# Optimization experiments

Measured on AMD Instinct MI355X. Metric: run time of the kernel, lower is better.

Reference implementation:

```python
import jax, jax.numpy as jnp
import numpy as np

B, N, D_MODEL, H = 2, 512, 256, 8
DH, DS, DE = 8, 8, 8          # hyperbolic / spherical / euclidean component dims
HEAD = D_MODEL // H           # 32
HALF = HEAD // 2              # 16 rope frequencies
KAPPA_S = 1.0                 # spherical curvature
EPS = 1e-6


def setup_inputs() -> dict:
    key = jax.random.key(0)
    ks = jax.random.split(key, 10)
    h = jax.random.normal(ks[0], (B, N, D_MODEL), jnp.float32)
    # manifold coords: hyperbolic part inside Poincare ball, spherical part on unit sphere
    xh = 0.3 * jnp.tanh(jax.random.normal(ks[1], (B, N, DH), jnp.float32))
    xs_raw = jax.random.normal(ks[2], (B, N, DS), jnp.float32)
    xs = xs_raw / jnp.linalg.norm(xs_raw, axis=-1, keepdims=True)
    xe = jax.random.normal(ks[3], (B, N, DE), jnp.float32)
    x = jnp.concatenate([xh, xs, xe], axis=-1)
    def lin(k):
        return 0.05 * jax.random.normal(k, (D_MODEL, D_MODEL), jnp.float32)
    inp = dict(
        h=h, x=x,
        Wq=lin(ks[4]), bq=jnp.zeros((D_MODEL,), jnp.float32),
        Wk=lin(ks[5]), bk=jnp.zeros((D_MODEL,), jnp.float32),
        Wv=lin(ks[6]), bv=jnp.zeros((D_MODEL,), jnp.float32),
        Wo=lin(ks[7]), bo=jnp.zeros((D_MODEL,), jnp.float32),
        w_kernel=jnp.ones((H, 3), jnp.float32),   # torch init: ones(num_heads, num_comp)
        beta=jnp.ones((H,), jnp.float32),
        edge_bias=0.1 * jax.random.normal(ks[8], (B, 1, N, N), jnp.float32),
        node_mask=jnp.ones((B, N), bool),
    )
    return inp


def _pairwise_geometry(x):
    """Returns dh (B,N,N), sdot (B,N,N), de2 (B,N,N), dist (B,N,N)."""
    xh, xs, xe = x[..., :DH], x[..., DH:DH + DS], x[..., DH + DS:]
    # hyperbolic: Poincare-ball distance arccosh(1 + 2|a-b|^2 / ((1-|a|^2)(1-|b|^2)))
    dh2_num = jnp.sum((xh[:, :, None, :] - xh[:, None, :, :]) ** 2, -1)
    one_m = 1.0 - jnp.sum(xh * xh, -1)                               # (B,N)
    arg = 1.0 + 2.0 * dh2_num / (one_m[:, :, None] * one_m[:, None, :])
    dh = jnp.arccosh(jnp.maximum(arg, 1.0 + EPS))
    # spherical: arccos of dot (unit vectors); raw dot kept for the kernel term
    sdot = jnp.einsum('bnd,bmd->bnm', xs, xs)
    ds = jnp.arccos(jnp.clip(sdot, -1.0 + EPS, 1.0 - EPS)) / np.sqrt(KAPPA_S)
    # euclidean: squared distance (kernel uses -d^2; product dist uses d^2)
    de2 = jnp.sum((xe[:, :, None, :] - xe[:, None, :, :]) ** 2, -1)
    dist = jnp.sqrt(dh * dh + ds * ds + de2)
    return dh, sdot, de2, dist


def reference(h, x, Wq, bq, Wk, bk, Wv, bv, Wo, bo, w_kernel, beta, edge_bias, node_mask):
    scale = 1.0 / np.sqrt(HEAD)
    rope_freq = jnp.exp(-np.log(10000.0) * jnp.arange(HALF, dtype=jnp.float32) / HALF)

    def heads(t):  # (B,N,D) -> (B,H,N,head)
        return t.reshape(B, N, H, HEAD).transpose(0, 2, 1, 3)

    Q = heads(h @ Wq.T + bq)
    K = heads(h @ Wk.T + bk)
    V = heads(h @ Wv.T + bv)

    dh, sdot, de2, dist = _pairwise_geometry(x)

    # M-RoPE: rotate Q by pairwise angle theta_ij = omega * d_M(x_i, x_j)
    theta = dist[..., None] * rope_freq                  # (B,N,N,half)
    cos_t = jnp.cos(theta)[:, None]                      # (B,1,N,N,half)
    sin_t = jnp.sin(theta)[:, None]
    q1, q2 = Q[..., 0::2], Q[..., 1::2]                  # (B,H,N,half)
    k1, k2 = K[..., 0::2], K[..., 1::2]
    qk_same = q1[:, :, :, None, :] * k1[:, :, None, :, :] + q2[:, :, :, None, :] * k2[:, :, None, :, :]
    qk_cross = q1[:, :, :, None, :] * k2[:, :, None, :, :] - q2[:, :, :, None, :] * k1[:, :, None, :, :]
    attn = (cos_t * qk_same + sin_t * qk_cross).sum(-1) * scale   # (B,H,N,N)

    # geodesic kernel bias: per-component kernels [H:-d_H, S:k*a.b, E:-|a-b|^2]
    kernel_stack = jnp.stack([-dh, KAPPA_S * sdot, -de2], axis=-1)  # (B,N,N,3)
    geo = jnp.einsum('hc,bnmc->bhnm', w_kernel, kernel_stack)
    attn = attn + beta[None, :, None, None] * geo + edge_bias

    attn = jnp.where(node_mask[:, None, None, :], attn, -jnp.inf)
    p = jax.nn.softmax(attn, axis=-1)
    out = jnp.einsum('bhnm,bhmd->bhnd', p, V).transpose(0, 2, 1, 3).reshape(B, N, D_MODEL)
    return out @ Wo.T + bo
```

## Files before the change

kernel.cpp:

```cpp
#include <hip/hip_runtime.h>

#define N_TOK 512
#define NH 8

typedef __attribute__((ext_vector_type(8))) short short8;
typedef __attribute__((ext_vector_type(4))) short short4v;
typedef __attribute__((ext_vector_type(4))) float f32x4;
typedef __attribute__((ext_vector_type(2))) _Float16 half2v;
typedef __attribute__((ext_vector_type(4))) _Float16 half4v;
typedef __attribute__((ext_vector_type(8))) _Float16 half8v;

__device__ __forceinline__ unsigned short f2bf(float f) {
    union { float f; unsigned u; } v; v.f = f;
    return (unsigned short)((v.u + 0x7FFF + ((v.u >> 16) & 1)) >> 16);
}

__global__ __launch_bounds__(256) void gemm_qkv_mfma(
    const float* __restrict__ A, const float* __restrict__ x,
    const float* __restrict__ Wq, const float* __restrict__ Wk, const float* __restrict__ Wv,
    const float* __restrict__ bq, const float* __restrict__ bk, const float* __restrict__ bv,
    float* __restrict__ Qb, _Float16* __restrict__ KT2, float* __restrict__ Vb,
    float* __restrict__ xT)
{
    const int bx = blockIdx.x;
    const int t = threadIdx.x;
    if (bx >= 768) {
        int idx = bx - 768;
        int b = idx / 24, k = idx % 24;
        const float* src = x + (size_t)b * 512 * 24 + k;
        float* dst = xT + (size_t)b * 12288 + k * 512;
        for (int j = t; j < 512; j += 256) dst[j] = src[j * 24];
        return;
    }
    const int z = bx >> 8, rem = bx & 255;
    const int m0 = (rem >> 3) * 32, n0 = (rem & 7) * 32;
    const float* W    = (z == 0) ? Wq : (z == 1) ? Wk : Wv;
    const float* bias = (z == 0) ? bq : (z == 1) ? bk : bv;

    __shared__ short As[32][264];
    __shared__ short Ws[32][264];

    #pragma unroll
    for (int r = 0; r < 8; ++r) {
        int idx = t + 256 * r;
        int row = idx >> 6, c4 = (idx & 63) * 4;
        float4 a = *(const float4*)&A[(m0 + row) * 256 + c4];
        short4v pa = {(short)f2bf(a.x), (short)f2bf(a.y), (short)f2bf(a.z), (short)f2bf(a.w)};
        *(short4v*)&As[row][c4] = pa;
        float4 w = *(const float4*)&W[(n0 + row) * 256 + c4];
        short4v pw = {(short)f2bf(w.x), (short)f2bf(w.y), (short)f2bf(w.z), (short)f2bf(w.w)};
        *(short4v*)&Ws[row][c4] = pw;
    }
    __syncthreads();

    const int w = t >> 6, lane = t & 63;
    const int wm = (w >> 1) * 16, wn = (w & 1) * 16;
    const int frow = lane & 15, kq = lane >> 4;

    f32x4 acc = {0.f, 0.f, 0.f, 0.f};
    #pragma unroll
    for (int k0 = 0; k0 < 8; ++k0) {
        short8 af = *(const short8*)&As[wm + frow][k0 * 32 + kq * 8];
        short8 wf = *(const short8*)&Ws[wn + frow][k0 * 32 + kq * 8];
        if (z == 1) acc = __builtin_amdgcn_mfma_f32_16x16x32_bf16(wf, af, acc, 0, 0, 0);
        else        acc = __builtin_amdgcn_mfma_f32_16x16x32_bf16(af, wf, acc, 0, 0, 0);
    }
    const int col = lane & 15, rq = (lane >> 4) * 4;
    if (z == 1) {
        int tok = m0 + wm + col;
        int bb = tok >> 9, jloc = tok & 511;
        #pragma unroll
        for (int r = 0; r < 4; ++r) {
            int d = n0 + wn + rq + r;
            KT2[(size_t)bb * 131072 + (size_t)(d >> 1) * 1024 + jloc * 2 + (d & 1)]
                = (_Float16)(acc[r] + bias[d]);
        }
    } else {
        float* C = (z == 0) ? Qb : Vb;
        const float sc = (z == 0) ? 0.17677669529663687f : 1.0f;
        float bsv = bias[n0 + wn + col];
        #pragma unroll
        for (int r = 0; r < 4; ++r)
            C[(m0 + wm + rq + r) * 256 + n0 + wn + col] = (acc[r] + bsv) * sc;
    }
}

__global__ __launch_bounds__(512, 4) void attn_kernel(
    const float* __restrict__ Q, const _Float16* __restrict__ KT2, const float* __restrict__ V,
    const float* __restrict__ x, const float* __restrict__ xT,
    const float* __restrict__ wker, const float* __restrict__ beta,
    const float* __restrict__ eb, float* __restrict__ Ao)
{
    const int i0 = blockIdx.x * 2;
    const int b  = blockIdx.y;
    const int t  = threadIdx.x;
    const int lane = t & 63;
    const int h = __builtin_amdgcn_readfirstlane(t >> 6);

    __shared__ half8v csn[16][2][64];
    __shared__ float es[2][NH][128];
    __shared__ float gdh[2][512], gsd[2][512], gde[2][512], gdist[2][512];

    {
        const float* xc = xT + (size_t)b * 12288 + t;
        float xv[24];
        #pragma unroll
        for (int k = 0; k < 24; ++k) xv[k] = xc[k * 512];
        float oj = 0.f;
        #pragma unroll
        for (int k = 0; k < 8; ++k) oj += xv[k] * xv[k];
        #pragma unroll
        for (int p = 0; p < 2; ++p) {
            const float* xi = x + (size_t)(b * N_TOK + i0 + p) * 24;
            float onemi = 1.0f, dh2 = 0.f, sd = 0.f, de2 = 0.f;
            #pragma unroll
            for (int k = 0; k < 8; ++k) {
                onemi -= xi[k] * xi[k];
                float d = xi[k] - xv[k]; dh2 += d * d;
            }
            #pragma unroll
            for (int k = 0; k < 8; ++k) sd += xi[8 + k] * xv[8 + k];
            #pragma unroll
            for (int k = 0; k < 8; ++k) { float d = xi[16 + k] - xv[16 + k]; de2 += d * d; }
            float arg = fmaf(2.0f * dh2, __builtin_amdgcn_rcpf(onemi * (1.0f - oj)), 1.0f);
            arg = fmaxf(arg, 1.0f + 1e-6f);
            float dh = __logf(arg + __builtin_amdgcn_sqrtf(fmaf(arg, arg, -1.0f)));
            float sdc = fminf(fmaxf(sd, -1.0f + 1e-6f), 1.0f - 1e-6f);
            float ax = fabsf(sdc);
            float pp = fmaf(ax, -0.0012624911f, 0.0066700901f);
            pp = fmaf(pp, ax, -0.0170881256f);
            pp = fmaf(pp, ax,  0.0308918810f);
            pp = fmaf(pp, ax, -0.0501743046f);
            pp = fmaf(pp, ax,  0.0889789874f);
            pp = fmaf(pp, ax, -0.2145988016f);
            pp = fmaf(pp, ax,  1.5707963050f);
            pp *= __builtin_amdgcn_sqrtf(1.0f - ax);
            float dsp = (sdc < 0.f) ? (3.14159265358979f - pp) : pp;
            float dist = __builtin_amdgcn_sqrtf(fmaf(dh, dh, fmaf(dsp, dsp, de2)));
            gdh[p][t] = dh; gsd[p][t] = sd; gde[p][t] = de2; gdist[p][t] = dist;
        }
    }

    const float* q0p = Q + (size_t)(b * N_TOK + i0) * 256 + h * 32;
    const float* q1p = q0p + 256;
    const float bet = beta[h];
    const float bw0 = bet * wker[h * 3 + 0], bw1 = bet * wker[h * 3 + 1], bw2 = bet * wker[h * 3 + 2];

    const int gjj = t & 127;
    const int gfh = __builtin_amdgcn_readfirstlane((t >> 7) & 1);
    const int gii = __builtin_amdgcn_readfirstlane(t >> 8);
    float frq[8];
    #pragma unroll
    for (int r = 0; r < 8; ++r)
        frq[r] = __expf(-0.5756462732485115f * (float)(gfh * 8 + r));

    float dsum[2] = {0.f, 0.f};
    float accv[2][4] = {{0.f,0.f,0.f,0.f},{0.f,0.f,0.f,0.f}};
    const int jsub = lane >> 3, dq = lane & 7;

    auto build = [&](int tile) {
        float d = gdist[gii][tile * 128 + gjj];
        #pragma unroll
        for (int r = 0; r < 8; ++r) {
            float sv, cv;
            __sincosf(d * frq[r], &sv, &cv);
            half4v p;
            p[0] = (_Float16)cv; p[1] = (_Float16)sv;
            p[2] = (_Float16)(-sv); p[3] = (_Float16)cv;
            ((half4v*)&csn[gfh * 8 + r][gii][gjj >> 1])[gjj & 1] = p;
        }
    };

    __syncthreads();
    build(0);
    const float* ebp0 = eb + ((size_t)b * N_TOK + i0) * N_TOK + 2 * lane;
    const float* ebp1 = ebp0 + N_TOK;
    float2 ebn0 = *(const float2*)ebp0;
    float2 ebn1 = *(const float2*)ebp1;
    __syncthreads();

    const _Float16* kbase = KT2 + (size_t)b * 131072 + (size_t)(h * 16) * 1024 + 4 * lane;

    for (int tile = 0; tile < 4; ++tile) {
        float2 eb0 = ebn0, eb1 = ebn1;
        if (tile < 3) {
            ebn0 = *(const float2*)(ebp0 + (tile + 1) * 128);
            ebn1 = *(const float2*)(ebp1 + (tile + 1) * 128);
        }
        {
            const _Float16* kp = kbase + tile * 256;
            half4v karr[16];
            #pragma unroll
            for (int f = 0; f < 16; ++f) karr[f] = *(const half4v*)(kp + f * 1024);

            float dot[2][2] = {{0.f, 0.f}, {0.f, 0.f}};
            #pragma unroll
            for (int f = 0; f < 16; ++f) {
                half2v k0 = {karr[f][0], karr[f][1]};
                half2v k1 = {karr[f][2], karr[f][3]};
                float q10 = q0p[2 * f], q20 = q0p[2 * f + 1];
                float q11 = q1p[2 * f], q21 = q1p[2 * f + 1];
                #pragma unroll
                for (int ii = 0; ii < 2; ++ii) {
                    half8v c8 = csn[f][ii][lane];
                    half2v cs0 = {c8[0], c8[1]}, rt0 = {c8[2], c8[3]};
                    half2v cs1 = {c8[4], c8[5]}, rt1 = {c8[6], c8[7]};
#if __has_builtin(__builtin_amdgcn_fdot2)
                    float u0 = __builtin_amdgcn_fdot2(cs0, k0, 0.f, false);
                    float v0 = __builtin_amdgcn_fdot2(rt0, k0, 0.f, false);
                    float u1 = __builtin_amdgcn_fdot2(cs1, k1, 0.f, false);
                    float v1 = __builtin_amdgcn_fdot2(rt1, k1, 0.f, false);
#else
                    float u0 = (float)cs0[0]*(float)k0[0] + (float)cs0[1]*(float)k0[1];
                    float v0 = (float)rt0[0]*(float)k0[0] + (float)rt0[1]*(float)k0[1];
                    float u1 = (float)cs1[0]*(float)k1[0] + (float)cs1[1]*(float)k1[1];
                    float v1 = (float)rt1[0]*(float)k1[0] + (float)rt1[1]*(float)k1[1];
#endif
                    float qa = ii ? q11 : q10, qb = ii ? q21 : q20;
                    dot[ii][0] = fmaf(qa, u0, fmaf(qb, v0, dot[ii][0]));
                    dot[ii][1] = fmaf(qa, u1, fmaf(qb, v1, dot[ii][1]));
                }
            }
            #pragma unroll
            for (int ii = 0; ii < 2; ++ii) {
                float2 g1 = *(const float2*)&gdh[ii][tile * 128 + 2 * lane];
                float2 g2 = *(const float2*)&gsd[ii][tile * 128 + 2 * lane];
                float2 g3 = *(const float2*)&gde[ii][tile * 128 + 2 * lane];
                float2 e2 = ii ? eb1 : eb0;
                float s0 = dot[ii][0] + (bw1 * g2.x - bw0 * g1.x - bw2 * g3.x) + e2.x;
                float s1 = dot[ii][1] + (bw1 * g2.y - bw0 * g1.y - bw2 * g3.y) + e2.y;
                float e0 = __expf(s0), e1 = __expf(s1);
                dsum[ii] += e0 + e1;
                *(float2*)&es[ii][h][2 * lane] = make_float2(e0, e1);
            }
        }
        if (tile < 3) { __syncthreads(); build(tile + 1); }
        {
            const float* vp = V + (size_t)(b * N_TOK + tile * 128 + jsub) * 256 + h * 32 + dq * 4;
            #pragma unroll
            for (int it = 0; it < 16; ++it) {
                float4 v4 = *(const float4*)(vp + it * 8 * 256);
                float e0 = es[0][h][it * 8 + jsub], e1 = es[1][h][it * 8 + jsub];
                accv[0][0] += e0 * v4.x; accv[0][1] += e0 * v4.y;
                accv[0][2] += e0 * v4.z; accv[0][3] += e0 * v4.w;
                accv[1][0] += e1 * v4.x; accv[1][1] += e1 * v4.y;
                accv[1][2] += e1 * v4.z; accv[1][3] += e1 * v4.w;
            }
        }
        if (tile < 3) __syncthreads();
    }

    #pragma unroll
    for (int ii = 0; ii < 2; ++ii) {
        float v = dsum[ii];
        v += __shfl_xor(v, 1);  v += __shfl_xor(v, 2);  v += __shfl_xor(v, 4);
        v += __shfl_xor(v, 8);  v += __shfl_xor(v, 16); v += __shfl_xor(v, 32);
        dsum[ii] = 1.0f / v;
    }
    #pragma unroll
    for (int ii = 0; ii < 2; ++ii)
        #pragma unroll
        for (int dd = 0; dd < 4; ++dd) {
            float a = accv[ii][dd];
            a += __shfl_xor(a, 8); a += __shfl_xor(a, 16); a += __shfl_xor(a, 32);
            accv[ii][dd] = a;
        }
    if (jsub == 0) {
        #pragma unroll
        for (int ii = 0; ii < 2; ++ii) {
            float4 o;
            o.x = accv[ii][0] * dsum[ii]; o.y = accv[ii][1] * dsum[ii];
            o.z = accv[ii][2] * dsum[ii]; o.w = accv[ii][3] * dsum[ii];
            *(float4*)&Ao[(size_t)(b * N_TOK + i0 + ii) * 256 + h * 32 + dq * 4] = o;
        }
    }
}

__global__ __launch_bounds__(256) void gemm_out_mfma(
    const float* __restrict__ Ao, const float* __restrict__ Wo,
    const float* __restrict__ bo, float* __restrict__ out)
{
    const int t = threadIdx.x;
    const int m0 = (blockIdx.x >> 3) * 32, n0 = (blockIdx.x & 7) * 32;

    __shared__ short As[32][264];
    __shared__ short Ws[32][264];

    #pragma unroll
    for (int r = 0; r < 8; ++r) {
        int idx = t + 256 * r;
        int row = idx >> 6, c4 = (idx & 63) * 4;
        float4 a = *(const float4*)&Ao[(m0 + row) * 256 + c4];
        short4v pa = {(short)f2bf(a.x), (short)f2bf(a.y), (short)f2bf(a.z), (short)f2bf(a.w)};
        *(short4v*)&As[row][c4] = pa;
        float4 w = *(const float4*)&Wo[(n0 + row) * 256 + c4];
        short4v pw = {(short)f2bf(w.x), (short)f2bf(w.y), (short)f2bf(w.z), (short)f2bf(w.w)};
        *(short4v*)&Ws[row][c4] = pw;
    }
    __syncthreads();

    const int w = t >> 6, lane = t & 63;
    const int wm = (w >> 1) * 16, wn = (w & 1) * 16;
    const int frow = lane & 15, kq = lane >> 4;

    f32x4 acc = {0.f, 0.f, 0.f, 0.f};
    #pragma unroll
    for (int k0 = 0; k0 < 8; ++k0) {
        short8 af = *(const short8*)&As[wm + frow][k0 * 32 + kq * 8];
        short8 wf = *(const short8*)&Ws[wn + frow][k0 * 32 + kq * 8];
        acc = __builtin_amdgcn_mfma_f32_16x16x32_bf16(af, wf, acc, 0, 0, 0);
    }
    const int col = lane & 15, rq = (lane >> 4) * 4;
    float bsv = bo[n0 + wn + col];
    #pragma unroll
    for (int r = 0; r < 4; ++r)
        out[(m0 + wm + rq + r) * 256 + n0 + wn + col] = acc[r] + bsv;
}

extern "C" void kernel_launch(void* const* d_in, const int* in_sizes, int n_in,
                              void* d_out, int out_size, void* d_ws, size_t ws_size,
                              hipStream_t stream) {
    const float* hin  = (const float*)d_in[0];
    const float* x    = (const float*)d_in[1];
    const float* Wq   = (const float*)d_in[2];
    const float* bq   = (const float*)d_in[3];
    const float* Wk   = (const float*)d_in[4];
    const float* bk   = (const float*)d_in[5];
    const float* Wv   = (const float*)d_in[6];
    const float* bv   = (const float*)d_in[7];
    const float* Wo   = (const float*)d_in[8];
    const float* bo   = (const float*)d_in[9];
    const float* wker = (const float*)d_in[10];
    const float* beta = (const float*)d_in[11];
    const float* eb   = (const float*)d_in[12];
    float* out = (float*)d_out;
    float* w   = (float*)d_ws;

    float*    Qb  = w;
    _Float16* KT2 = (_Float16*)(w + 262144);
    float*    Vb  = w + 393216;
    float*    Ao  = w + 655360;
    float*    xT  = w + 917504;

    hipLaunchKernelGGL(gemm_qkv_mfma, dim3(816), dim3(256), 0, stream,
                       hin, x, Wq, Wk, Wv, bq, bk, bv, Qb, KT2, Vb, xT);
    hipLaunchKernelGGL(attn_kernel, dim3(256, 2), dim3(512), 0, stream,
                       Qb, KT2, Vb, x, xT, wker, beta, eb, Ao);
    hipLaunchKernelGGL(gemm_out_mfma, dim3(256), dim3(256), 0, stream,
                       Ao, Wo, bo, out);
}
```

Measured before the change: 121.6 us.

## Halve cos/sin LDS table, rebuild swapped K pairs, raise attention occupancy

The rotation table in shared memory now stores only (cos, sin) per entry instead of (cos, sin, -sin, cos). The second dot product reuses it by building a swapped, negated K pair in registers. K loads are split into two groups of eight to lower register pressure, and launch bounds are raised from 4 to 8 blocks per CU. This cuts LDS footprint and traffic and aims for higher occupancy, at the cost of extra register shuffles and possible spills under the tighter register cap.

```diff
diff --git a/kernel.cpp b/kernel.cpp
--- a/kernel.cpp
+++ b/kernel.cpp
@@ -8,7 +8,6 @@
 typedef __attribute__((ext_vector_type(4))) float f32x4;
 typedef __attribute__((ext_vector_type(2))) _Float16 half2v;
 typedef __attribute__((ext_vector_type(4))) _Float16 half4v;
-typedef __attribute__((ext_vector_type(8))) _Float16 half8v;
 
 __device__ __forceinline__ unsigned short f2bf(float f) {
     union { float f; unsigned u; } v; v.f = f;
@@ -85,7 +84,7 @@
     }
 }
 
-__global__ __launch_bounds__(512, 4) void attn_kernel(
+__global__ __launch_bounds__(512, 8) void attn_kernel(
     const float* __restrict__ Q, const _Float16* __restrict__ KT2, const float* __restrict__ V,
     const float* __restrict__ x, const float* __restrict__ xT,
     const float* __restrict__ wker, const float* __restrict__ beta,
@@ -97,7 +96,7 @@
     const int lane = t & 63;
     const int h = __builtin_amdgcn_readfirstlane(t >> 6);
 
-    __shared__ half8v csn[16][2][64];
+    __shared__ half2v csn[16][2][128];
     __shared__ float es[2][NH][128];
     __shared__ float gdh[2][512], gsd[2][512], gde[2][512], gdist[2][512];
 
@@ -164,10 +163,8 @@
         for (int r = 0; r < 8; ++r) {
             float sv, cv;
             __sincosf(d * frq[r], &sv, &cv);
-            half4v p;
-            p[0] = (_Float16)cv; p[1] = (_Float16)sv;
-            p[2] = (_Float16)(-sv); p[3] = (_Float16)cv;
-            ((half4v*)&csn[gfh * 8 + r][gii][gjj >> 1])[gjj & 1] = p;
+            half2v p; p[0] = (_Float16)cv; p[1] = (_Float16)sv;
+            csn[gfh * 8 + r][gii][gjj] = p;
         }
     };
 
@@ -188,37 +185,41 @@
             ebn1 = *(const float2*)(ebp1 + (tile + 1) * 128);
         }
         {
-            const _Float16* kp = kbase + tile * 256;
-            half4v karr[16];
-            #pragma unroll
-            for (int f = 0; f < 16; ++f) karr[f] = *(const half4v*)(kp + f * 1024);
-
             float dot[2][2] = {{0.f, 0.f}, {0.f, 0.f}};
             #pragma unroll
-            for (int f = 0; f < 16; ++f) {
-                half2v k0 = {karr[f][0], karr[f][1]};
-                half2v k1 = {karr[f][2], karr[f][3]};
-                float q10 = q0p[2 * f], q20 = q0p[2 * f + 1];
-                float q11 = q1p[2 * f], q21 = q1p[2 * f + 1];
+            for (int fg = 0; fg < 2; ++fg) {
+                const _Float16* kp = kbase + tile * 256 + (size_t)fg * 8 * 1024;
+                half4v karr[8];
                 #pragma unroll
-                for (int ii = 0; ii < 2; ++ii) {
-                    half8v c8 = csn[f][ii][lane];
-                    half2v cs0 = {c8[0], c8[1]}, rt0 = {c8[2], c8[3]};
-                    half2v cs1 = {c8[4], c8[5]}, rt1 = {c8[6], c8[7]};
+                for (int fl = 0; fl < 8; ++fl) karr[fl] = *(const half4v*)(kp + fl * 1024);
+                #pragma unroll
+                for (int fl = 0; fl < 8; ++fl) {
+                    const int f = fg * 8 + fl;
+                    half2v k0  = {karr[fl][0], karr[fl][1]};
+                    half2v k1  = {karr[fl][2], karr[fl][3]};
+                    half2v ks0 = {karr[fl][1], -karr[fl][0]};
+                    half2v ks1 = {karr[fl][3], -karr[fl][2]};
+                    float q10 = q0p[2 * f], q20 = q0p[2 * f + 1];
+                    float q11 = q1p[2 * f], q21 = q1p[2 * f + 1];
+                    #pragma unroll
+                    for (int ii = 0; ii < 2; ++ii) {
+                        half4v cc = *(const half4v*)&csn[f][ii][2 * lane];
+                        half2v cs0 = {cc[0], cc[1]}, cs1 = {cc[2], cc[3]};
 #if __has_builtin(__builtin_amdgcn_fdot2)
-                    float u0 = __builtin_amdgcn_fdot2(cs0, k0, 0.f, false);
-                    float v0 = __builtin_amdgcn_fdot2(rt0, k0, 0.f, false);
-                    float u1 = __builtin_amdgcn_fdot2(cs1, k1, 0.f, false);
-                    float v1 = __builtin_amdgcn_fdot2(rt1, k1, 0.f, false);
+                        float u0 = __builtin_amdgcn_fdot2(cs0, k0,  0.f, false);
+                        float v0 = __builtin_amdgcn_fdot2(cs0, ks0, 0.f, false);
+                        float u1 = __builtin_amdgcn_fdot2(cs1, k1,  0.f, false);
+                        float v1 = __builtin_amdgcn_fdot2(cs1, ks1, 0.f, false);
 #else
-                    float u0 = (float)cs0[0]*(float)k0[0] + (float)cs0[1]*(float)k0[1];
-                    float v0 = (float)rt0[0]*(float)k0[0] + (float)rt0[1]*(float)k0[1];
-                    float u1 = (float)cs1[0]*(float)k1[0] + (float)cs1[1]*(float)k1[1];
-                    float v1 = (float)rt1[0]*(float)k1[0] + (float)rt1[1]*(float)k1[1];
+                        float u0 = (float)cs0[0]*(float)k0[0] + (float)cs0[1]*(float)k0[1];
+                        float v0 = (float)cs0[0]*(float)ks0[0] + (float)cs0[1]*(float)ks0[1];
+                        float u1 = (float)cs1[0]*(float)k1[0] + (float)cs1[1]*(float)k1[1];
+                        float v1 = (float)cs1[0]*(float)ks1[0] + (float)cs1[1]*(float)ks1[1];
 #endif
-                    float qa = ii ? q11 : q10, qb = ii ? q21 : q20;
-                    dot[ii][0] = fmaf(qa, u0, fmaf(qb, v0, dot[ii][0]));
-                    dot[ii][1] = fmaf(qa, u1, fmaf(qb, v1, dot[ii][1]));
+                        float qa = ii ? q11 : q10, qb = ii ? q21 : q20;
+                        dot[ii][0] = fmaf(qa, u0, fmaf(qb, v0, dot[ii][0]));
+                        dot[ii][1] = fmaf(qa, u1, fmaf(qb, v1, dot[ii][1]));
+                    }
                 }
             }
             #pragma unroll
```

Result: slower. 206.2 us (+69.6%).
